# Optimization experiments

Hardware: AMD Instinct MI355X
Metric: run time of the kernel (lower is better)

## Reference

```python
import jax, jax.numpy as jnp
import numpy as np

B, T, D_MODEL, N_HEADS, N_KV = 2, 2048, 1024, 16, 4
HEAD = D_MODEL // N_HEADS  # 64
NEG_INF = -1e9


def sine_table(features, length):
    # standard RoPE frequency table: theta_i = 10000^(2i/d)
    fraction = jnp.arange(0, features, 2, dtype=jnp.float32) / features
    timescale = 10000.0 ** fraction  # (features/2,)
    sinusoid = jnp.arange(length, dtype=jnp.float32)[:, None] / timescale[None, :]
    sinusoid = jnp.concatenate([sinusoid, sinusoid], axis=-1)  # (L, features)
    return jnp.sin(sinusoid), jnp.cos(sinusoid)


def rotate_half(x):
    x1, x2 = jnp.split(x, 2, axis=-1)
    return jnp.concatenate([-x2, x1], axis=-1)


def apply_rope(x, sin, cos):
    # x: (B, H, T, D); sin/cos: (L, D)
    t = x.shape[-2]
    return x * cos[:t][None, None] + rotate_half(x) * sin[:t][None, None]


def setup_inputs() -> dict:
    key = jax.random.key(0)
    k1, k2, k3, k4 = jax.random.split(key, 4)
    return {
        'q': jax.random.normal(k1, (B, T, D_MODEL), dtype=jnp.float32),
        'k': jax.random.normal(k2, (B, T, N_KV * HEAD), dtype=jnp.float32),
        'v': jax.random.normal(k3, (B, T, N_KV * HEAD), dtype=jnp.float32),
        'w_out': jax.random.normal(k4, (D_MODEL, D_MODEL), dtype=jnp.float32) * 0.02,
    }


def reference(q, k, v, w_out):
    Bq, Tq, C = q.shape
    head = C // N_HEADS
    # split heads: q -> (B, n_heads, T, head); k/v -> (B, n_kv, T, head)
    qh = q.reshape(Bq, Tq, N_HEADS, head).transpose(0, 2, 1, 3)
    kh = k.reshape(Bq, Tq, N_KV, head).transpose(0, 2, 1, 3)
    vh = v.reshape(Bq, Tq, N_KV, head).transpose(0, 2, 1, 3)
    # inline RoPE on q and k
    sin, cos = sine_table(head, Tq)
    qh = apply_rope(qh, sin, cos)
    kh = apply_rope(kh, sin, cos)
    # GQA repeat of kv heads to match q heads
    rep = N_HEADS // N_KV
    kh = jnp.repeat(kh, rep, axis=1)
    vh = jnp.repeat(vh, rep, axis=1)
    # manual scaled-dot-product attention with causal masking (full T^2 logits)
    logits = jnp.einsum('bhqd,bhkd->bhqk', qh, kh) / jnp.sqrt(jnp.float32(head))
    causal = jnp.tril(jnp.ones((Tq, Tq), dtype=jnp.float32))
    logits = jnp.where(causal == 0, NEG_INF, logits)
    attn = jax.nn.softmax(logits, axis=-1)
    out = jnp.einsum('bhqk,bhkd->bhqd', attn, vh)
    out = out.transpose(0, 2, 1, 3).reshape(Bq, Tq, C)
    return out @ w_out
```

## Files before the change

### kernel.cpp

```cpp
#include <hip/hip_runtime.h>
#include <math.h>

#define T_SEQ 2048
#define NH    16
#define NKV   4

typedef __attribute__((ext_vector_type(8)))  _Float16 f16x8;
typedef __attribute__((ext_vector_type(4)))  _Float16 f16x4;
typedef __attribute__((ext_vector_type(2)))  __fp16   fp16x2b;
typedef __attribute__((ext_vector_type(4)))  float    f32x4;
typedef __attribute__((ext_vector_type(16))) float    f32x16;

#if __has_builtin(__builtin_amdgcn_exp2f)
#define EXP2F(x) __builtin_amdgcn_exp2f(x)
#else
#define EXP2F(x) exp2f(x)
#endif

#define QSCALE 0.18033688011112042f

#define LDS_BARRIER()                                        \
    do {                                                     \
        __builtin_amdgcn_sched_barrier(0);                   \
        asm volatile("s_waitcnt lgkmcnt(0)" ::: "memory");   \
        __builtin_amdgcn_s_barrier();                        \
        __builtin_amdgcn_sched_barrier(0);                   \
    } while (0)

__global__ __launch_bounds__(256) void prep_kernel(const float* __restrict__ k,
                                                   const float* __restrict__ v,
                                                   const float* __restrict__ w,
                                                   float2* __restrict__ tb,
                                                   _Float16* __restrict__ Kr,
                                                   _Float16* __restrict__ Vt,
                                                   _Float16* __restrict__ Wt)
{
    __shared__ _Float16 L[64 * 72];
    const int bx = blockIdx.x;
    if (bx < 256) {
        int idx = bx * 256 + threadIdx.x;
        int i = idx & 31, t = idx >> 5;
        float inv = __expf((float)i * (-9.210340371976184f / 32.0f));
        float ang = (float)t * inv;
        tb[idx] = make_float2(cosf(ang), sinf(ang));
    } else if (bx < 2304) {
        int idx = (bx - 256) * 256 + threadIdx.x;
        int i   = idx & 31;
        int t   = (idx >> 5) & 2047;
        int bk  = idx >> 16;
        float inv = __expf((float)i * (-9.210340371976184f / 32.0f));
        float ang = (float)t * inv;
        float sn = sinf(ang), cs = cosf(ang);
        const float* src = k + ((size_t)(bk >> 2) * T_SEQ + t) * 256 + (bk & 3) * 64 + i;
        float x1 = src[0], x2 = src[32];
        _Float16* dst = Kr + ((size_t)bk * T_SEQ + t) * 64 + i;
        dst[0]  = (_Float16)(x1 * cs - x2 * sn);
        dst[32] = (_Float16)(x2 * cs + x1 * sn);
    } else if (bx < 2560) {
        const int id = bx - 2304;
        const int t0 = (id & 31) * 64, bk = id >> 5;
        const int b = bk >> 2, kh = bk & 3;
        const int rr = threadIdx.x >> 2, pp = threadIdx.x & 3;
        const float* src = v + ((size_t)(b * T_SEQ + t0 + rr)) * 256 + kh * 64 + pp * 16;
        f32x4 s0 = *(const f32x4*)(src), s1 = *(const f32x4*)(src + 4);
        f32x4 s2 = *(const f32x4*)(src + 8), s3 = *(const f32x4*)(src + 12);
        _Float16* lp = &L[rr * 72 + pp * 16];
        #pragma unroll
        for (int j = 0; j < 4; ++j) { lp[j] = (_Float16)s0[j]; lp[4+j] = (_Float16)s1[j];
                                      lp[8+j] = (_Float16)s2[j]; lp[12+j] = (_Float16)s3[j]; }
        __syncthreads();
        f16x8 w0, w1;
        #pragma unroll
        for (int j = 0; j < 8; ++j) w0[j] = L[(pp * 16 + j) * 72 + rr];
        #pragma unroll
        for (int j = 0; j < 8; ++j) w1[j] = L[(pp * 16 + 8 + j) * 72 + rr];
        _Float16* dst = Vt + ((size_t)bk * 64 + rr) * T_SEQ + t0 + pp * 16;
        *(f16x8*)dst = w0; *(f16x8*)(dst + 8) = w1;
    } else {
        const int id = bx - 2560;
        const int k0 = (id & 15) * 64, n0 = (id >> 4) * 64;
        const int rr = threadIdx.x >> 2, pp = threadIdx.x & 3;
        const float* src = w + (size_t)(k0 + rr) * 1024 + n0 + pp * 16;
        f32x4 s0 = *(const f32x4*)(src), s1 = *(const f32x4*)(src + 4);
        f32x4 s2 = *(const f32x4*)(src + 8), s3 = *(const f32x4*)(src + 12);
        _Float16* lp = &L[rr * 72 + pp * 16];
        #pragma unroll
        for (int j = 0; j < 4; ++j) { lp[j] = (_Float16)s0[j]; lp[4+j] = (_Float16)s1[j];
                                      lp[8+j] = (_Float16)s2[j]; lp[12+j] = (_Float16)s3[j]; }
        __syncthreads();
        f16x8 w0, w1;
        #pragma unroll
        for (int j = 0; j < 8; ++j) w0[j] = L[(pp * 16 + j) * 72 + rr];
        #pragma unroll
        for (int j = 0; j < 8; ++j) w1[j] = L[(pp * 16 + 8 + j) * 72 + rr];
        _Float16* dst = Wt + (size_t)(n0 + rr) * 1024 + k0 + pp * 16;
        *(f16x8*)dst = w0; *(f16x8*)(dst + 8) = w1;
    }
}


__global__ __launch_bounds__(256) void attn_kernel(const float* __restrict__ q,
                                                   const float2* __restrict__ tb,
                                                   const _Float16* __restrict__ Kr,
                                                   const _Float16* __restrict__ Vt,
                                                   _Float16* __restrict__ AO)
{
    __shared__ _Float16 smem[16384];

    const int tid  = threadIdx.x;
    const int wid  = tid >> 6;
    const int lane = tid & 63;
    const int bid = blockIdx.x;
    const int c   = (bid < 256) ? (15 - (bid >> 5)) : ((bid - 256) >> 5);
    const int bh  = bid & 31;
    const int b = bh >> 4, h = bh & 15;
    const int bkh = b * NKV + (h >> 2);
    const int hi = lane >> 5;
    const int qc = lane & 31;
    const int qlo = c * 128 + wid * 32;
    const int tq  = qlo + qc;
    const int NT  = 2 * c + 2;

    const int srow   = wid * 16 + (lane >> 3);
    const int schunk = lane & 7;
    const _Float16* kgbase = Kr + (size_t)bkh * T_SEQ * 64;
    const _Float16* vgbase = Vt + (size_t)bkh * 64 * T_SEQ;
    const int kd0 = srow * 64 + ((schunk ^ (srow & 7)) * 8);
    const int kd1 = kd0 + 8 * 64;

    f16x8 sAK0, sAK1, sAV0, sAV1, sBK0, sBK1, sBV0, sBV1;
    {
        const _Float16* kg = kgbase + (size_t)srow * 64 + schunk * 8;
        sAK0 = *(const f16x8*)(kg);
        sAK1 = *(const f16x8*)(kg + 8 * 64);
        const _Float16* vg = vgbase + (size_t)srow * T_SEQ + schunk * 8;
        sAV0 = *(const f16x8*)(vg);
        sAV1 = *(const f16x8*)(vg + 8 * T_SEQ);
    }

    f16x8 qa[4];
    {
        const float* qrow = q + ((size_t)b * T_SEQ + tq) * 1024 + h * 64;
        float raw[4][8];
        #pragma unroll
        for (int ds = 0; ds < 4; ++ds) {
            f32x4 r0 = *(const f32x4*)(qrow + 16 * ds + 8 * hi);
            f32x4 r1 = *(const f32x4*)(qrow + 16 * ds + 8 * hi + 4);
            #pragma unroll
            for (int j = 0; j < 4; ++j) { raw[ds][j] = r0[j]; raw[ds][4 + j] = r1[j]; }
        }
        #pragma unroll
        for (int ds = 0; ds < 2; ++ds) {
            const float2* tp = tb + (size_t)tq * 32 + 16 * ds + 8 * hi;
            #pragma unroll
            for (int j = 0; j < 8; ++j) {
                float2 cs = tp[j];
                float x0 = raw[ds][j], x1 = raw[ds + 2][j];
                qa[ds][j]     = (_Float16)((x0 * cs.x - x1 * cs.y) * QSCALE);
                qa[ds + 2][j] = (_Float16)((x1 * cs.x + x0 * cs.y) * QSCALE);
            }
        }
    }

    *(f16x8*)(&smem[kd0])        = sAK0;
    *(f16x8*)(&smem[kd1])        = sAK1;
    *(f16x8*)(&smem[8192 + kd0]) = sAV0;
    *(f16x8*)(&smem[8192 + kd1]) = sAV1;
    {
        const _Float16* kg = kgbase + (size_t)(64 + srow) * 64 + schunk * 8;
        sBK0 = *(const f16x8*)(kg);
        sBK1 = *(const f16x8*)(kg + 8 * 64);
        const _Float16* vg = vgbase + (size_t)srow * T_SEQ + 64 + schunk * 8;
        sBV0 = *(const f16x8*)(vg);
        sBV1 = *(const f16x8*)(vg + 8 * T_SEQ);
    }
    LDS_BARRIER();

    f32x16 o0, o1;
    #pragma unroll
    for (int i = 0; i < 16; ++i) { o0[i] = 0.f; o1[i] = 0.f; }
    float mrun = -INFINITY, lsum = 0.0f;

    auto tile_body = [&](int kvb,
                         f16x8& iK0, f16x8& iK1, f16x8& iV0, f16x8& iV1,
                         f16x8& oK0, f16x8& oK1, f16x8& oV0, f16x8& oV1) {
        if (kvb + 2 < NT) {
            const int nb = (kvb + 2) * 64;
            const _Float16* kg = kgbase + (size_t)(nb + srow) * 64 + schunk * 8;
            iK0 = *(const f16x8*)(kg);
            iK1 = *(const f16x8*)(kg + 8 * 64);
            const _Float16* vg = vgbase + (size_t)srow * T_SEQ + nb + schunk * 8;
            iV0 = *(const f16x8*)(vg);
            iV1 = *(const f16x8*)(vg + 8 * T_SEQ);
        }
        const _Float16* ks = smem + (kvb & 1) * 4096;
        const _Float16* vs = smem + 8192 + (kvb & 1) * 4096;

        const int rel = kvb * 64 - qlo;
        if (rel <= 0) {
            const bool act1 = (rel <= -32);
            f32x16 s0, s1;
            #pragma unroll
            for (int i = 0; i < 16; ++i) { s0[i] = 0.f; s1[i] = 0.f; }
            __builtin_amdgcn_s_setprio(1);
            {
                const int krow = qc;
                const int rsw = krow & 7;
                #pragma unroll
                for (int ds = 0; ds < 4; ++ds) {
                    f16x8 ka = *(const f16x8*)(ks + krow * 64 + (((2*ds + hi) ^ rsw) * 8));
                    s0 = __builtin_amdgcn_mfma_f32_32x32x16_f16(ka, qa[ds], s0, 0, 0, 0);
                }
            }
            if (act1) {
                const int krow = 32 + qc;
                const int rsw = krow & 7;
                #pragma unroll
                for (int ds = 0; ds < 4; ++ds) {
                    f16x8 ka = *(const f16x8*)(ks + krow * 64 + (((2*ds + hi) ^ rsw) * 8));
                    s1 = __builtin_amdgcn_mfma_f32_32x32x16_f16(ka, qa[ds], s1, 0, 0, 0);
                }
            }
            __builtin_amdgcn_s_setprio(0);

            if (rel == 0) {
                #pragma unroll
                for (int r = 0; r < 16; ++r)
                    if ((r & 3) + 8 * (r >> 2) + 4 * hi > qc) s0[r] = -1e30f;
            }
            if (act1 && rel == -32) {
                #pragma unroll
                for (int r = 0; r < 16; ++r)
                    if ((r & 3) + 8 * (r >> 2) + 4 * hi > qc) s1[r] = -1e30f;
            }

            float pmL = s0[0];
            #pragma unroll
            for (int r = 1; r < 16; ++r) pmL = fmaxf(pmL, s0[r]);
            if (act1) {
                #pragma unroll
                for (int r = 0; r < 16; ++r) pmL = fmaxf(pmL, s1[r]);
            }
            if (!__all(pmL <= mrun + 8.0f)) {
                float pm = fmaxf(pmL, __shfl_xor(pmL, 32));
                float mn = fmaxf(mrun, pm);
                float corr = EXP2F(mrun - mn);
                mrun = mn;
                lsum *= corr;
                #pragma unroll
                for (int r = 0; r < 16; ++r) {
                    float cfr = __shfl(corr, (r & 3) + 8 * (r >> 2) + 4 * hi);
                    o0[r] *= cfr; o1[r] *= cfr;
                }
            }

            unsigned pk0[8], pk1[8];
            float ps = 0.0f;
            #pragma unroll
            for (int i = 0; i < 8; ++i) {
                float p0 = EXP2F(s0[2*i]     - mrun);
                float p1 = EXP2F(s0[2*i + 1] - mrun);
                ps += p0 + p1;
                union { fp16x2b hh; unsigned u; } cv;
                cv.hh = __builtin_amdgcn_cvt_pkrtz(p0, p1);
                pk0[i] = cv.u;
            }
            if (act1) {
                #pragma unroll
                for (int i = 0; i < 8; ++i) {
                    float p0 = EXP2F(s1[2*i]     - mrun);
                    float p1 = EXP2F(s1[2*i + 1] - mrun);
                    ps += p0 + p1;
                    union { fp16x2b hh; unsigned u; } cv;
                    cv.hh = __builtin_amdgcn_cvt_pkrtz(p0, p1);
                    pk1[i] = cv.u;
                }
            }
            lsum += ps;

            union { unsigned u[4]; f16x8 v; } af[4];
            {
                unsigned t0 = (unsigned)__shfl_xor((int)(hi ? pk0[0] : pk0[2]), 32);
                unsigned t1 = (unsigned)__shfl_xor((int)(hi ? pk0[1] : pk0[3]), 32);
                unsigned t2 = (unsigned)__shfl_xor((int)(hi ? pk0[4] : pk0[6]), 32);
                unsigned t3 = (unsigned)__shfl_xor((int)(hi ? pk0[5] : pk0[7]), 32);
                af[0].u[0] = hi ? t0 : pk0[0]; af[0].u[1] = hi ? t1 : pk0[1];
                af[0].u[2] = hi ? pk0[2] : t0; af[0].u[3] = hi ? pk0[3] : t1;
                af[1].u[0] = hi ? t2 : pk0[4]; af[1].u[1] = hi ? t3 : pk0[5];
                af[1].u[2] = hi ? pk0[6] : t2; af[1].u[3] = hi ? pk0[7] : t3;
            }
            if (act1) {
                unsigned t0 = (unsigned)__shfl_xor((int)(hi ? pk1[0] : pk1[2]), 32);
                unsigned t1 = (unsigned)__shfl_xor((int)(hi ? pk1[1] : pk1[3]), 32);
                unsigned t2 = (unsigned)__shfl_xor((int)(hi ? pk1[4] : pk1[6]), 32);
                unsigned t3 = (unsigned)__shfl_xor((int)(hi ? pk1[5] : pk1[7]), 32);
                af[2].u[0] = hi ? t0 : pk1[0]; af[2].u[1] = hi ? t1 : pk1[1];
                af[2].u[2] = hi ? pk1[2] : t0; af[2].u[3] = hi ? pk1[3] : t1;
                af[3].u[0] = hi ? t2 : pk1[4]; af[3].u[1] = hi ? t3 : pk1[5];
                af[3].u[2] = hi ? pk1[6] : t2; af[3].u[3] = hi ? pk1[7] : t3;
            }

            __builtin_amdgcn_s_setprio(1);
            const int nkc = act1 ? 4 : 2;
            #pragma unroll
            for (int kc = 0; kc < 4; ++kc) {
                if (kc < nkc) {
                    const int vr0 = qc;
                    const int vr1 = 32 + qc;
                    f16x8 vb0 = *(const f16x8*)(vs + vr0 * 64 + (((2*kc + hi) ^ (vr0 & 7)) * 8));
                    f16x8 vb1 = *(const f16x8*)(vs + vr1 * 64 + (((2*kc + hi) ^ (vr1 & 7)) * 8));
                    o0 = __builtin_amdgcn_mfma_f32_32x32x16_f16(af[kc].v, vb0, o0, 0, 0, 0);
                    o1 = __builtin_amdgcn_mfma_f32_32x32x16_f16(af[kc].v, vb1, o1, 0, 0, 0);
                }
            }
            __builtin_amdgcn_s_setprio(0);
        }

        if (kvb + 1 < NT) {
            _Float16* kw = smem + ((kvb + 1) & 1) * 4096;
            _Float16* vw = smem + 8192 + ((kvb + 1) & 1) * 4096;
            *(f16x8*)(&kw[kd0]) = oK0;
            *(f16x8*)(&kw[kd1]) = oK1;
            *(f16x8*)(&vw[kd0]) = oV0;
            *(f16x8*)(&vw[kd1]) = oV1;
        }
        LDS_BARRIER();
    };

    for (int t = 0; t < NT; ) {
        tile_body(t, sAK0, sAK1, sAV0, sAV1, sBK0, sBK1, sBV0, sBV1); ++t;
        if (t >= NT) break;
        tile_body(t, sBK0, sBK1, sBV0, sBV1, sAK0, sAK1, sAV0, sAV1); ++t;
    }

    lsum += __shfl_xor(lsum, 32);
    const float li = 1.0f / lsum;
    __syncthreads();
    {
        _Float16* Os = smem;
        #pragma unroll
        for (int r = 0; r < 16; ++r) {
            const int crow = (r & 3) + 8 * (r >> 2) + 4 * hi;
            float lir = __shfl(li, crow);
            Os[(wid * 32 + crow) * 72 + qc]      = (_Float16)(o0[r] * lir);
            Os[(wid * 32 + crow) * 72 + 32 + qc] = (_Float16)(o1[r] * lir);
        }
    }
    __syncthreads();
    {
        const int row = tid >> 1, part = tid & 1;
        const _Float16* src = smem + row * 72 + part * 32;
        _Float16* dst = AO + ((size_t)b * T_SEQ + c * 128 + row) * 1024 + h * 64 + part * 32;
        #pragma unroll
        for (int j = 0; j < 4; ++j)
            *(f16x8*)(dst + j * 8) = *(const f16x8*)(src + j * 8);
    }
}


#define AST 40
__global__ __launch_bounds__(256) void gemm_kernel(const _Float16* __restrict__ A,
                                                   const _Float16* __restrict__ Bt,
                                                   float* __restrict__ C)
{
    __shared__ _Float16 As[2][128 * AST];
    __shared__ _Float16 Bs[2][64 * AST];
    const int tid  = threadIdx.x;
    const int by   = blockIdx.x & 31;
    const int bx   = blockIdx.x >> 5;
    const int lane = tid & 63;
    const int wid  = tid >> 6;
    const int g = lane >> 4, r = lane & 15;
    const int wm = wid >> 1, wn = wid & 1;

    f32x4 acc[4][2];
    #pragma unroll
    for (int i = 0; i < 4; ++i)
        #pragma unroll
        for (int j = 0; j < 2; ++j) acc[i][j] = (f32x4){0.f,0.f,0.f,0.f};

    const int c0 = tid, c1 = tid + 256;
    const size_t a0off = (size_t)(by*128 + (c0 >> 2)) * 1024 + (c0 & 3) * 8;
    const size_t a1off = (size_t)(by*128 + (c1 >> 2)) * 1024 + (c1 & 3) * 8;
    const size_t b0off = (size_t)(bx*64  + (c0 >> 2)) * 1024 + (c0 & 3) * 8;
    const int ad0 = (c0 >> 2) * AST + (c0 & 3) * 8;
    const int ad1 = (c1 >> 2) * AST + (c1 & 3) * 8;

    f16x8 a0 = *(const f16x8*)(A  + a0off);
    f16x8 a1 = *(const f16x8*)(A  + a1off);
    f16x8 b0 = *(const f16x8*)(Bt + b0off);
    *(f16x8*)(&As[0][ad0]) = a0;
    *(f16x8*)(&As[0][ad1]) = a1;
    *(f16x8*)(&Bs[0][ad0]) = b0;
    __syncthreads();
    int cur = 0;

    for (int kt = 0; kt < 32; ++kt) {
        if (kt < 31) {
            a0 = *(const f16x8*)(A  + a0off + (kt+1) * 32);
            a1 = *(const f16x8*)(A  + a1off + (kt+1) * 32);
            b0 = *(const f16x8*)(Bt + b0off + (kt+1) * 32);
        }
        f16x8 af[4], bfv[2];
        #pragma unroll
        for (int mi = 0; mi < 4; ++mi)
            af[mi] = *(const f16x8*)(&As[cur][(wm*64 + mi*16 + r) * AST + 8 * g]);
        #pragma unroll
        for (int ni = 0; ni < 2; ++ni)
            bfv[ni] = *(const f16x8*)(&Bs[cur][(wn*32 + ni*16 + r) * AST + 8 * g]);
        __builtin_amdgcn_s_setprio(1);
        #pragma unroll
        for (int mi = 0; mi < 4; ++mi)
            #pragma unroll
            for (int ni = 0; ni < 2; ++ni)
                acc[mi][ni] = __builtin_amdgcn_mfma_f32_16x16x32_f16(
                                  af[mi], bfv[ni], acc[mi][ni], 0, 0, 0);
        __builtin_amdgcn_s_setprio(0);
        if (kt < 31) {
            *(f16x8*)(&As[cur ^ 1][ad0]) = a0;
            *(f16x8*)(&As[cur ^ 1][ad1]) = a1;
            *(f16x8*)(&Bs[cur ^ 1][ad0]) = b0;
            cur ^= 1;
        }
        __syncthreads();
    }
    #pragma unroll
    for (int mi = 0; mi < 4; ++mi)
        #pragma unroll
        for (int ni = 0; ni < 2; ++ni)
            #pragma unroll
            for (int j = 0; j < 4; ++j)
                C[(size_t)(by*128 + wm*64 + mi*16 + 4*g + j) * 1024
                  + bx*64 + wn*32 + ni*16 + r] = acc[mi][ni][j];
}


extern "C" void kernel_launch(void* const* d_in, const int* in_sizes, int n_in,
                              void* d_out, int out_size, void* d_ws, size_t ws_size,
                              hipStream_t stream) {
    const float* q = (const float*)d_in[0];
    const float* k = (const float*)d_in[1];
    const float* v = (const float*)d_in[2];
    const float* w = (const float*)d_in[3];
    float* out = (float*)d_out;

    char* ws = (char*)d_ws;
    float2*   tb = (float2*)(ws);
    _Float16* Kr = (_Float16*)(ws + ((size_t)1 << 20));
    _Float16* Vt = (_Float16*)(ws + ((size_t)3 << 20));
    _Float16* Wt = (_Float16*)(ws + ((size_t)5 << 20));
    _Float16* AO = (_Float16*)(ws + ((size_t)7 << 20));

    hipLaunchKernelGGL(prep_kernel,  dim3(2816), dim3(256), 0, stream, k, v, w, tb, Kr, Vt, Wt);
    hipLaunchKernelGGL(attn_kernel,  dim3(512),  dim3(256), 0, stream, q, tb, Kr, Vt, AO);
    hipLaunchKernelGGL(gemm_kernel,  dim3(512),  dim3(256), 0, stream, AO, Wt, out);
}
```

Baseline: 79.98 us.

## Pair short and long causal query chunks per block for balanced attention work

Each attention block now handles two 64-row query chunks: waves 0-1 take chunk p and waves 2-3 take chunk 31-p. Every block therefore walks a similar number of KV tiles (32-p), replacing the old scheme that ordered 128-row blocks from longest to shortest. The QK MFMAs for the two key halves are interleaved, and the max and sum reductions are split into independent chains to shorten dependencies. The catch is that the waves within a block now do uneven work, since the short-chunk waves stay idle for many tiles while still joining the shared barriers.

```diff
diff --git a/kernel.cpp b/kernel.cpp
--- a/kernel.cpp
+++ b/kernel.cpp
@@ -111,15 +111,16 @@
     const int wid  = tid >> 6;
     const int lane = tid & 63;
     const int bid = blockIdx.x;
-    const int c   = (bid < 256) ? (15 - (bid >> 5)) : ((bid - 256) >> 5);
-    const int bh  = bid & 31;
+    const int p   = bid & 15;
+    const int bh  = bid >> 4;
     const int b = bh >> 4, h = bh & 15;
     const int bkh = b * NKV + (h >> 2);
     const int hi = lane >> 5;
     const int qc = lane & 31;
-    const int qlo = c * 128 + wid * 32;
+    const int chunk = (wid < 2) ? p : (31 - p);
+    const int qlo = chunk * 64 + (wid & 1) * 32;
     const int tq  = qlo + qc;
-    const int NT  = 2 * c + 2;
+    const int NT  = 32 - p;
 
     const int srow   = wid * 16 + (lane >> 3);
     const int schunk = lane & 7;
@@ -166,7 +167,7 @@
     *(f16x8*)(&smem[kd1])        = sAK1;
     *(f16x8*)(&smem[8192 + kd0]) = sAV0;
     *(f16x8*)(&smem[8192 + kd1]) = sAV1;
-    {
+    if (NT > 1) {
         const _Float16* kg = kgbase + (size_t)(64 + srow) * 64 + schunk * 8;
         sBK0 = *(const f16x8*)(kg);
         sBK1 = *(const f16x8*)(kg + 8 * 64);
@@ -204,21 +205,16 @@
             for (int i = 0; i < 16; ++i) { s0[i] = 0.f; s1[i] = 0.f; }
             __builtin_amdgcn_s_setprio(1);
             {
-                const int krow = qc;
-                const int rsw = krow & 7;
+                const int r0 = qc, rsw0 = qc & 7;
+                const int r1 = 32 + qc;
                 #pragma unroll
                 for (int ds = 0; ds < 4; ++ds) {
-                    f16x8 ka = *(const f16x8*)(ks + krow * 64 + (((2*ds + hi) ^ rsw) * 8));
-                    s0 = __builtin_amdgcn_mfma_f32_32x32x16_f16(ka, qa[ds], s0, 0, 0, 0);
-                }
-            }
-            if (act1) {
-                const int krow = 32 + qc;
-                const int rsw = krow & 7;
-                #pragma unroll
-                for (int ds = 0; ds < 4; ++ds) {
-                    f16x8 ka = *(const f16x8*)(ks + krow * 64 + (((2*ds + hi) ^ rsw) * 8));
-                    s1 = __builtin_amdgcn_mfma_f32_32x32x16_f16(ka, qa[ds], s1, 0, 0, 0);
+                    f16x8 ka0 = *(const f16x8*)(ks + r0 * 64 + (((2*ds + hi) ^ rsw0) * 8));
+                    s0 = __builtin_amdgcn_mfma_f32_32x32x16_f16(ka0, qa[ds], s0, 0, 0, 0);
+                    if (act1) {
+                        f16x8 ka1 = *(const f16x8*)(ks + r1 * 64 + (((2*ds + hi) ^ rsw0) * 8));
+                        s1 = __builtin_amdgcn_mfma_f32_32x32x16_f16(ka1, qa[ds], s1, 0, 0, 0);
+                    }
                 }
             }
             __builtin_amdgcn_s_setprio(0);
@@ -234,13 +230,17 @@
                     if ((r & 3) + 8 * (r >> 2) + 4 * hi > qc) s1[r] = -1e30f;
             }
 
-            float pmL = s0[0];
-            #pragma unroll
-            for (int r = 1; r < 16; ++r) pmL = fmaxf(pmL, s0[r]);
+            float mt[8];
+            #pragma unroll
+            for (int i = 0; i < 8; ++i) mt[i] = fmaxf(s0[2*i], s0[2*i+1]);
             if (act1) {
                 #pragma unroll
-                for (int r = 0; r < 16; ++r) pmL = fmaxf(pmL, s1[r]);
-            }
+                for (int i = 0; i < 8; ++i)
+                    mt[i] = fmaxf(mt[i], fmaxf(s1[2*i], s1[2*i+1]));
+            }
+            #pragma unroll
+            for (int i = 0; i < 4; ++i) mt[i] = fmaxf(mt[i], mt[i+4]);
+            float pmL = fmaxf(fmaxf(mt[0], mt[1]), fmaxf(mt[2], mt[3]));
             if (!__all(pmL <= mrun + 8.0f)) {
                 float pm = fmaxf(pmL, __shfl_xor(pmL, 32));
                 float mn = fmaxf(mrun, pm);
@@ -255,12 +255,12 @@
             }
 
             unsigned pk0[8], pk1[8];
-            float ps = 0.0f;
+            float psa = 0.0f, psb = 0.0f;
             #pragma unroll
             for (int i = 0; i < 8; ++i) {
                 float p0 = EXP2F(s0[2*i]     - mrun);
                 float p1 = EXP2F(s0[2*i + 1] - mrun);
-                ps += p0 + p1;
+                psa += p0; psb += p1;
                 union { fp16x2b hh; unsigned u; } cv;
                 cv.hh = __builtin_amdgcn_cvt_pkrtz(p0, p1);
                 pk0[i] = cv.u;
@@ -270,13 +270,13 @@
                 for (int i = 0; i < 8; ++i) {
                     float p0 = EXP2F(s1[2*i]     - mrun);
                     float p1 = EXP2F(s1[2*i + 1] - mrun);
-                    ps += p0 + p1;
+                    psa += p0; psb += p1;
                     union { fp16x2b hh; unsigned u; } cv;
                     cv.hh = __builtin_amdgcn_cvt_pkrtz(p0, p1);
                     pk1[i] = cv.u;
                 }
             }
-            lsum += ps;
+            lsum += psa + psb;
 
             union { unsigned u[4]; f16x8 v; } af[4];
             {
@@ -349,8 +349,11 @@
     __syncthreads();
     {
         const int row = tid >> 1, part = tid & 1;
+        const int wsrc = row >> 5;
+        const int chs  = (wsrc < 2) ? p : (31 - p);
+        const int grow = chs * 64 + (wsrc & 1) * 32 + (row & 31);
         const _Float16* src = smem + row * 72 + part * 32;
-        _Float16* dst = AO + ((size_t)b * T_SEQ + c * 128 + row) * 1024 + h * 64 + part * 32;
+        _Float16* dst = AO + ((size_t)b * T_SEQ + grow) * 1024 + h * 64 + part * 32;
         #pragma unroll
         for (int j = 0; j < 4; ++j)
             *(f16x8*)(dst + j * 8) = *(const f16x8*)(src + j * 8);
```

Result: slower. 92.96 us (+16.2%).
